# Optimization experiments

Hardware: AMD Instinct MI355X
Metric: run time of the kernel (lower is better)

The kernel has to match this reference:

```python
import jax, jax.numpy as jnp
import numpy as np

C = 256
DK = C // 8  # query/key channels


def setup_inputs() -> dict:
    key = jax.random.key(0)
    ks = jax.random.split(key, 7)
    B, W, H = 4, 64, 64
    x = jax.random.normal(ks[0], (B, C, W, H), dtype=jnp.float32)
    s_in = 1.0 / np.sqrt(C)
    Wq = jax.random.normal(ks[1], (DK, C), dtype=jnp.float32) * s_in
    bq = jnp.zeros((DK,), dtype=jnp.float32)
    Wk = jax.random.normal(ks[2], (DK, C), dtype=jnp.float32) * s_in
    bk = jnp.zeros((DK,), dtype=jnp.float32)
    Wv = jax.random.normal(ks[3], (C, C), dtype=jnp.float32) * s_in
    bv = jnp.zeros((C,), dtype=jnp.float32)
    return {"x": x, "Wq": Wq, "bq": bq, "Wk": Wk, "bk": bk, "Wv": Wv, "bv": bv}


def reference(x, Wq, bq, Wk, bk, Wv, bv):
    B, Cc, W, H = x.shape
    N = W * H
    xf = x.reshape(B, Cc, N)  # (B, C, N) flattened spatial
    # 1x1 convs == channel matmuls
    q = jnp.einsum('dc,bcn->bnd', Wq, xf) + bq  # (B, N, DK)
    k = jnp.einsum('dc,bcn->bdn', Wk, xf) + bk[None, :, None]  # (B, DK, N)
    v = jnp.einsum('oc,bcn->bon', Wv, xf) + bv[None, :, None]  # (B, C, N)
    energy = jnp.einsum('bnd,bdm->bnm', q, k) / jnp.sqrt(jnp.float32(q.shape[-1]))
    attn = jax.nn.softmax(energy, axis=-1)  # (B, N, N)
    out = jnp.einsum('bcn,bmn->bcm', v, attn)  # v @ attn^T
    return out.reshape(B, Cc, W, H) + x
```

## Files before the change

### kernel.cpp

```cpp
#include <hip/hip_runtime.h>
#include <hip/hip_bf16.h>
#include <math.h>

#define BB 4
#define CC 256
#define DKK 32
#define NN 4096
#define QSCALE 0.2550181864060454f

typedef __attribute__((ext_vector_type(8))) __bf16 bf16x8;
typedef __attribute__((ext_vector_type(4))) __bf16 bf16x4;
typedef __attribute__((ext_vector_type(4))) float f32x4;
typedef __attribute__((ext_vector_type(16))) float f32x16;

#define XST 260
#define SCRST 33

__global__ __launch_bounds__(256, 2) void qkv_kernel(
    const float* __restrict__ x,
    const float* __restrict__ Wq, const float* __restrict__ bq,
    const float* __restrict__ Wk, const float* __restrict__ bk,
    const float* __restrict__ Wv, const float* __restrict__ bv,
    __bf16* __restrict__ qws, __bf16* __restrict__ kws, __bf16* __restrict__ vws)
{
    __shared__ __align__(16) unsigned char smem[16640];
    __bf16* xsT = (__bf16*)smem;
    float*  scr = (float*)smem;

    const int tid = threadIdx.x;
    const int w   = tid >> 6;
    const int l   = tid & 63;
    const int l15 = l & 15;
    const int lq  = l >> 4;
    const int n0  = blockIdx.x * 32;
    const int b   = blockIdx.y;

    {
        const int cb = tid >> 3;
        const int nf = (tid & 7) * 4;
        const float* xp = x + ((size_t)(b * CC) + cb) * NN + n0 + nf;
#pragma unroll
        for (int r = 0; r < 8; r++) {
            float4 v = *(const float4*)(xp + (size_t)r * 32 * NN);
            int c = r * 32 + cb;
            xsT[(nf + 0) * XST + c] = (__bf16)v.x;
            xsT[(nf + 1) * XST + c] = (__bf16)v.y;
            xsT[(nf + 2) * XST + c] = (__bf16)v.z;
            xsT[(nf + 3) * XST + c] = (__bf16)v.w;
        }
    }

    const float* wp[5];
#pragma unroll
    for (int ot = 0; ot < 5; ot++) {
        int ob = 80 * w + 16 * ot;
        const float* src = (ob < 32) ? (Wq + (size_t)ob * CC)
                         : (ob < 64) ? (Wk + (size_t)(ob - 32) * CC)
                                     : (Wv + (size_t)(ob - 64) * CC);
        wp[ot] = src + (size_t)l15 * CC;
    }

    float4 wc[5][2], wn[5][2];
#pragma unroll
    for (int ot = 0; ot < 5; ot++) {
        wc[ot][0] = *(const float4*)(wp[ot] + lq * 8);
        wc[ot][1] = *(const float4*)(wp[ot] + lq * 8 + 4);
    }

    __syncthreads();

    const f32x4 zf = {0.f, 0.f, 0.f, 0.f};
    f32x4 acc[5][2];
#pragma unroll
    for (int i = 0; i < 5; i++)
#pragma unroll
        for (int j = 0; j < 2; j++) acc[i][j] = zf;

#pragma unroll
    for (int ks = 0; ks < 8; ks++) {
        if (ks < 7) {
#pragma unroll
            for (int ot = 0; ot < 5; ot++) {
                wn[ot][0] = *(const float4*)(wp[ot] + (ks + 1) * 32 + lq * 8);
                wn[ot][1] = *(const float4*)(wp[ot] + (ks + 1) * 32 + lq * 8 + 4);
            }
        }
        bf16x8 bfr[2];
#pragma unroll
        for (int nt = 0; nt < 2; nt++) {
            bf16x4 lo = *(const bf16x4*)&xsT[(nt * 16 + l15) * XST + ks * 32 + lq * 8];
            bf16x4 hi = *(const bf16x4*)&xsT[(nt * 16 + l15) * XST + ks * 32 + lq * 8 + 4];
            bfr[nt] = __builtin_shufflevector(lo, hi, 0, 1, 2, 3, 4, 5, 6, 7);
        }
#pragma unroll
        for (int ot = 0; ot < 5; ot++) {
            bf16x8 af;
            af[0] = (__bf16)wc[ot][0].x; af[1] = (__bf16)wc[ot][0].y;
            af[2] = (__bf16)wc[ot][0].z; af[3] = (__bf16)wc[ot][0].w;
            af[4] = (__bf16)wc[ot][1].x; af[5] = (__bf16)wc[ot][1].y;
            af[6] = (__bf16)wc[ot][1].z; af[7] = (__bf16)wc[ot][1].w;
#pragma unroll
            for (int nt = 0; nt < 2; nt++)
                acc[ot][nt] = __builtin_amdgcn_mfma_f32_16x16x32_bf16(af, bfr[nt], acc[ot][nt], 0, 0, 0);
        }
        if (ks < 7) {
#pragma unroll
            for (int ot = 0; ot < 5; ot++) { wc[ot][0] = wn[ot][0]; wc[ot][1] = wn[ot][1]; }
        }
    }

    __syncthreads();

    __bf16* vchunk = vws + (size_t)b * CC * NN + (size_t)(n0 >> 5) * 8192;
#pragma unroll
    for (int ot = 0; ot < 5; ot++) {
        int ob = 80 * w + ot * 16;
#pragma unroll
        for (int nt = 0; nt < 2; nt++) {
#pragma unroll
            for (int r = 0; r < 4; r++) {
                int o = ob + lq * 4 + r;
                int n = nt * 16 + l15;
                float val = acc[ot][nt][r];
                if (ob >= 64) {
                    int c = o - 64;
                    vchunk[(c >> 5) * 1024 + nt * 512 + (c & 31) * 16 + l15] =
                        (__bf16)(val + bv[c]);
                } else if (ob < 32) {
                    scr[o * SCRST + n] = (val + bq[o]) * QSCALE;
                } else {
                    scr[o * SCRST + n] = val + bk[o - 32];
                }
            }
        }
    }
    __syncthreads();
    {
        int n  = tid >> 3;
        int d0 = (tid & 7) * 4;
        bf16x4 qv, kv;
#pragma unroll
        for (int j = 0; j < 4; j++) {
            qv[j] = (__bf16)scr[(d0 + j) * SCRST + n];
            kv[j] = (__bf16)scr[(32 + d0 + j) * SCRST + n];
        }
        size_t base = ((size_t)b * NN + n0 + n) * DKK + d0;
        *(bf16x4*)&qws[base] = qv;
        *(bf16x4*)&kws[base] = kv;
    }
}

#define PST 36
#define MST 68
#define PWSZ (64 * PST)

__global__ __launch_bounds__(256, 2) void attn_kernel(
    const __bf16* __restrict__ qb, const __bf16* __restrict__ kb,
    const __bf16* __restrict__ vt, const float* __restrict__ x,
    float* __restrict__ out)
{
    __shared__ __align__(16) unsigned char smem[38144];
    __bf16* pw   = (__bf16*)smem + (threadIdx.x >> 6) * 2 * PWSZ;
    float*  Ls   = (float*)(smem + 36864);
    float*  Linv = (float*)(smem + 37888);

    const int tid = threadIdx.x;
    const int w   = tid >> 6;
    const int l   = tid & 63;
    const int l15 = l & 15;
    const int lq  = l >> 4;
    const int l31 = l & 31;
    const int lh  = l >> 5;

    const int beta = blockIdx.x;
    const int b    = (beta >> 1) & 3;
    const int ch   = (beta >> 3) & 1;
    const int mt   = ((beta >> 4) << 1) | (beta & 1);
    const int m0   = mt * 64;

    const __bf16* qbb = qb + (size_t)b * NN * DKK;
    const __bf16* kbb = kb + (size_t)b * NN * DKK;
    const __bf16* vtb = vt + (size_t)b * CC * NN;

    bf16x8 qa[4];
#pragma unroll
    for (int af = 0; af < 4; af++)
        qa[af] = *(const bf16x8*)(qbb + (size_t)(m0 + af * 16 + l15) * DKK + lq * 8);

    const __bf16* kstrip = kbb + (size_t)(w * 32 + l15) * DKK + lq * 8;
    const __bf16* vstrip = vtb + (size_t)w * 8192 + (size_t)ch * 4096
                               + l31 * 16 + lh * 8;

    const f32x4  zf  = {0.f, 0.f, 0.f, 0.f};
    f32x16 acc32[2][4];
    {
        const f32x16 z16 = {0.f,0.f,0.f,0.f,0.f,0.f,0.f,0.f,
                            0.f,0.f,0.f,0.f,0.f,0.f,0.f,0.f};
#pragma unroll
        for (int i = 0; i < 2; i++)
#pragma unroll
            for (int j = 0; j < 4; j++) acc32[i][j] = z16;
    }
    float lacc[4] = {0.f, 0.f, 0.f, 0.f};

    bf16x8 kA0 = *(const bf16x8*)kstrip;
    bf16x8 kA1 = *(const bf16x8*)(kstrip + 16 * DKK);
#pragma unroll
    for (int af = 0; af < 4; af++) {
        f32x4 e0 = __builtin_amdgcn_mfma_f32_16x16x32_bf16(kA0, qa[af], zf, 0, 0, 0);
        f32x4 e1 = __builtin_amdgcn_mfma_f32_16x16x32_bf16(kA1, qa[af], zf, 0, 0, 0);
        bf16x4 p0, p1;
#pragma unroll
        for (int r = 0; r < 4; r++) {
            float v0 = __builtin_amdgcn_exp2f(e0[r]); lacc[af] += v0; p0[r] = (__bf16)v0;
            float v1 = __builtin_amdgcn_exp2f(e1[r]); lacc[af] += v1; p1[r] = (__bf16)v1;
        }
        *(bf16x4*)&pw[(af * 16 + l15) * PST + lq * 4]      = p0;
        *(bf16x4*)&pw[(af * 16 + l15) * PST + 16 + lq * 4] = p1;
    }
    kA0 = *(const bf16x8*)(kstrip + (size_t)128 * DKK);
    kA1 = *(const bf16x8*)(kstrip + (size_t)144 * DKK);

#pragma unroll 2
    for (int ic = 0; ic < 31; ic++) {
        const int cur = ic & 1;
        const __bf16* vch = vstrip + (size_t)ic * 32768;

        bf16x8 vf[4][2];
#pragma unroll
        for (int ct = 0; ct < 4; ct++) {
            vf[ct][0] = *(const bf16x8*)(vch + ct * 1024);
            vf[ct][1] = *(const bf16x8*)(vch + ct * 1024 + 512);
        }

        bf16x8 pf[2][2];
#pragma unroll
        for (int mt2 = 0; mt2 < 2; mt2++)
#pragma unroll
            for (int ks = 0; ks < 2; ks++) {
                const __bf16* pr = &pw[cur * PWSZ + (mt2 * 32 + l31) * PST + ks * 16 + lh * 8];
                bf16x4 plo = *(const bf16x4*)pr;
                bf16x4 phi = *(const bf16x4*)(pr + 4);
                pf[mt2][ks] = __builtin_shufflevector(plo, phi, 0, 1, 2, 3, 4, 5, 6, 7);
            }

#pragma unroll
        for (int af = 0; af < 4; af++) {
            f32x4 e0 = __builtin_amdgcn_mfma_f32_16x16x32_bf16(kA0, qa[af], zf, 0, 0, 0);
            f32x4 e1 = __builtin_amdgcn_mfma_f32_16x16x32_bf16(kA1, qa[af], zf, 0, 0, 0);
            bf16x4 p0, p1;
#pragma unroll
            for (int r = 0; r < 4; r++) {
                float v0 = __builtin_amdgcn_exp2f(e0[r]); lacc[af] += v0; p0[r] = (__bf16)v0;
                float v1 = __builtin_amdgcn_exp2f(e1[r]); lacc[af] += v1; p1[r] = (__bf16)v1;
            }
            *(bf16x4*)&pw[(cur ^ 1) * PWSZ + (af * 16 + l15) * PST + lq * 4]      = p0;
            *(bf16x4*)&pw[(cur ^ 1) * PWSZ + (af * 16 + l15) * PST + 16 + lq * 4] = p1;
        }
        kA0 = *(const bf16x8*)(kstrip + (size_t)(ic + 2) * 128 * DKK);
        kA1 = *(const bf16x8*)(kstrip + (size_t)((ic + 2) * 128 + 16) * DKK);

#pragma unroll
        for (int mt2 = 0; mt2 < 2; mt2++)
#pragma unroll
            for (int ct = 0; ct < 4; ct++) {
                acc32[mt2][ct] = __builtin_amdgcn_mfma_f32_32x32x16_bf16(
                    vf[ct][0], pf[mt2][0], acc32[mt2][ct], 0, 0, 0);
                acc32[mt2][ct] = __builtin_amdgcn_mfma_f32_32x32x16_bf16(
                    vf[ct][1], pf[mt2][1], acc32[mt2][ct], 0, 0, 0);
            }
    }

    {
        const __bf16* vch = vstrip + (size_t)31 * 32768;
        bf16x8 vf[4][2];
#pragma unroll
        for (int ct = 0; ct < 4; ct++) {
            vf[ct][0] = *(const bf16x8*)(vch + ct * 1024);
            vf[ct][1] = *(const bf16x8*)(vch + ct * 1024 + 512);
        }
        bf16x8 pf[2][2];
#pragma unroll
        for (int mt2 = 0; mt2 < 2; mt2++)
#pragma unroll
            for (int ks = 0; ks < 2; ks++) {
                const __bf16* pr = &pw[(31 & 1) * PWSZ + (mt2 * 32 + l31) * PST + ks * 16 + lh * 8];
                bf16x4 plo = *(const bf16x4*)pr;
                bf16x4 phi = *(const bf16x4*)(pr + 4);
                pf[mt2][ks] = __builtin_shufflevector(plo, phi, 0, 1, 2, 3, 4, 5, 6, 7);
            }
#pragma unroll
        for (int mt2 = 0; mt2 < 2; mt2++)
#pragma unroll
            for (int ct = 0; ct < 4; ct++) {
                acc32[mt2][ct] = __builtin_amdgcn_mfma_f32_32x32x16_bf16(
                    vf[ct][0], pf[mt2][0], acc32[mt2][ct], 0, 0, 0);
                acc32[mt2][ct] = __builtin_amdgcn_mfma_f32_32x32x16_bf16(
                    vf[ct][1], pf[mt2][1], acc32[mt2][ct], 0, 0, 0);
            }
    }

#pragma unroll
    for (int af = 0; af < 4; af++) {
        lacc[af] += __shfl_xor(lacc[af], 16, 64);
        lacc[af] += __shfl_xor(lacc[af], 32, 64);
    }
    if (lq == 0) {
#pragma unroll
        for (int af = 0; af < 4; af++) Ls[w * 64 + af * 16 + l15] = lacc[af];
    }
    __syncthreads();
    if (tid < 64)
        Linv[tid] = 1.0f / (Ls[tid] + Ls[64 + tid] + Ls[128 + tid] + Ls[192 + tid]);

    float* Ored = (float*)smem + w * (32 * MST);
#pragma unroll
    for (int q = 0; q < 4; q++) {
        if (q > 0) __syncthreads();
#pragma unroll
        for (int mt2 = 0; mt2 < 2; mt2++) {
#pragma unroll
            for (int reg = 0; reg < 16; reg++) {
                int row = (reg & 3) + 8 * (reg >> 2) + 4 * lh;
                Ored[row * MST + mt2 * 32 + l31] = acc32[mt2][q][reg];
            }
        }
        __syncthreads();
        const int cl  = tid >> 3;
        const int mi0 = (tid & 7) * 8;
        const float* Ob = (const float*)smem + cl * MST;
#pragma unroll
        for (int j = 0; j < 2; j++) {
            int mi = mi0 + 4 * j;
            f32x4 s = *(const f32x4*)&Ob[mi];
            s = s + *(const f32x4*)&Ob[1 * (32 * MST) + mi];
            s = s + *(const f32x4*)&Ob[2 * (32 * MST) + mi];
            s = s + *(const f32x4*)&Ob[3 * (32 * MST) + mi];
            f32x4 li = *(const f32x4*)&Linv[mi];
            int c = ch * 128 + q * 32 + cl;
            size_t gi = ((size_t)(b * CC + c)) * NN + m0 + mi;
            f32x4 xr = *(const f32x4*)&x[gi];
            *(f32x4*)&out[gi] = s * li + xr;
        }
    }
}

extern "C" void kernel_launch(void* const* d_in, const int* in_sizes, int n_in,
                              void* d_out, int out_size, void* d_ws, size_t ws_size,
                              hipStream_t stream) {
    const float* x  = (const float*)d_in[0];
    const float* Wq = (const float*)d_in[1];
    const float* bq = (const float*)d_in[2];
    const float* Wk = (const float*)d_in[3];
    const float* bk = (const float*)d_in[4];
    const float* Wv = (const float*)d_in[5];
    const float* bv = (const float*)d_in[6];
    float* out = (float*)d_out;

    __bf16* qws = (__bf16*)d_ws;
    __bf16* kws = qws + (size_t)BB * NN * DKK;
    __bf16* vws = kws + (size_t)BB * NN * DKK;

    qkv_kernel<<<dim3(128, BB), 256, 0, stream>>>(x, Wq, bq, Wk, bk, Wv, bv,
                                                  qws, kws, vws);
    attn_kernel<<<dim3(512), 256, 0, stream>>>(qws, kws, vws, x, out);
}
```

Measured before the change: 152.5 us.

## Keep softmax probabilities in registers by matching QK^T MFMA output to PV input layout

```diff
diff --git a/kernel.cpp b/kernel.cpp
--- a/kernel.cpp
+++ b/kernel.cpp
@@ -111,6 +111,7 @@
 
     __syncthreads();
 
+    const int voff = ((l15 >> 2) & 1) * 8 + (l15 & 3) + ((l15 >> 3) & 1) * 4;
     __bf16* vchunk = vws + (size_t)b * CC * NN + (size_t)(n0 >> 5) * 8192;
 #pragma unroll
     for (int ot = 0; ot < 5; ot++) {
@@ -124,7 +125,7 @@
                 float val = acc[ot][nt][r];
                 if (ob >= 64) {
                     int c = o - 64;
-                    vchunk[(c >> 5) * 1024 + nt * 512 + (c & 31) * 16 + l15] =
+                    vchunk[(c >> 5) * 1024 + nt * 512 + (c & 31) * 16 + voff] =
                         (__bf16)(val + bv[c]);
                 } else if (ob < 32) {
                     scr[o * SCRST + n] = (val + bq[o]) * QSCALE;
@@ -150,25 +151,20 @@
     }
 }
 
-#define PST 36
 #define MST 68
-#define PWSZ (64 * PST)
 
 __global__ __launch_bounds__(256, 2) void attn_kernel(
     const __bf16* __restrict__ qb, const __bf16* __restrict__ kb,
     const __bf16* __restrict__ vt, const float* __restrict__ x,
     float* __restrict__ out)
 {
-    __shared__ __align__(16) unsigned char smem[38144];
-    __bf16* pw   = (__bf16*)smem + (threadIdx.x >> 6) * 2 * PWSZ;
-    float*  Ls   = (float*)(smem + 36864);
-    float*  Linv = (float*)(smem + 37888);
+    __shared__ __align__(16) unsigned char smem[36096];
+    float* Ls   = (float*)(smem + 34816);
+    float* Linv = (float*)(smem + 35840);
 
     const int tid = threadIdx.x;
     const int w   = tid >> 6;
     const int l   = tid & 63;
-    const int l15 = l & 15;
-    const int lq  = l >> 4;
     const int l31 = l & 31;
     const int lh  = l >> 5;
 
@@ -182,48 +178,32 @@
     const __bf16* kbb = kb + (size_t)b * NN * DKK;
     const __bf16* vtb = vt + (size_t)b * CC * NN;
 
-    bf16x8 qa[4];
-#pragma unroll
-    for (int af = 0; af < 4; af++)
-        qa[af] = *(const bf16x8*)(qbb + (size_t)(m0 + af * 16 + l15) * DKK + lq * 8);
-
-    const __bf16* kstrip = kbb + (size_t)(w * 32 + l15) * DKK + lq * 8;
+    bf16x8 qa[2][2];
+#pragma unroll
+    for (int mt2 = 0; mt2 < 2; mt2++)
+#pragma unroll
+        for (int kc = 0; kc < 2; kc++)
+            qa[mt2][kc] = *(const bf16x8*)(qbb + (size_t)(m0 + mt2 * 32 + l31) * DKK
+                                           + kc * 16 + lh * 8);
+
+    const __bf16* kstrip = kbb + (size_t)(w * 32 + l31) * DKK + lh * 8;
     const __bf16* vstrip = vtb + (size_t)w * 8192 + (size_t)ch * 4096
                                + l31 * 16 + lh * 8;
 
-    const f32x4  zf  = {0.f, 0.f, 0.f, 0.f};
+    const f32x16 z16 = {0.f,0.f,0.f,0.f,0.f,0.f,0.f,0.f,
+                        0.f,0.f,0.f,0.f,0.f,0.f,0.f,0.f};
     f32x16 acc32[2][4];
-    {
-        const f32x16 z16 = {0.f,0.f,0.f,0.f,0.f,0.f,0.f,0.f,
-                            0.f,0.f,0.f,0.f,0.f,0.f,0.f,0.f};
-#pragma unroll
-        for (int i = 0; i < 2; i++)
-#pragma unroll
-            for (int j = 0; j < 4; j++) acc32[i][j] = z16;
-    }
-    float lacc[4] = {0.f, 0.f, 0.f, 0.f};
-
-    bf16x8 kA0 = *(const bf16x8*)kstrip;
-    bf16x8 kA1 = *(const bf16x8*)(kstrip + 16 * DKK);
-#pragma unroll
-    for (int af = 0; af < 4; af++) {
-        f32x4 e0 = __builtin_amdgcn_mfma_f32_16x16x32_bf16(kA0, qa[af], zf, 0, 0, 0);
-        f32x4 e1 = __builtin_amdgcn_mfma_f32_16x16x32_bf16(kA1, qa[af], zf, 0, 0, 0);
-        bf16x4 p0, p1;
-#pragma unroll
-        for (int r = 0; r < 4; r++) {
-            float v0 = __builtin_amdgcn_exp2f(e0[r]); lacc[af] += v0; p0[r] = (__bf16)v0;
-            float v1 = __builtin_amdgcn_exp2f(e1[r]); lacc[af] += v1; p1[r] = (__bf16)v1;
-        }
-        *(bf16x4*)&pw[(af * 16 + l15) * PST + lq * 4]      = p0;
-        *(bf16x4*)&pw[(af * 16 + l15) * PST + 16 + lq * 4] = p1;
-    }
-    kA0 = *(const bf16x8*)(kstrip + (size_t)128 * DKK);
-    kA1 = *(const bf16x8*)(kstrip + (size_t)144 * DKK);
+#pragma unroll
+    for (int i = 0; i < 2; i++)
+#pragma unroll
+        for (int j = 0; j < 4; j++) acc32[i][j] = z16;
+    float lacc[2] = {0.f, 0.f};
+
+    bf16x8 kf0 = *(const bf16x8*)kstrip;
+    bf16x8 kf1 = *(const bf16x8*)(kstrip + 16);
 
 #pragma unroll 2
-    for (int ic = 0; ic < 31; ic++) {
-        const int cur = ic & 1;
+    for (int ic = 0; ic < 32; ic++) {
         const __bf16* vch = vstrip + (size_t)ic * 32768;
 
         bf16x8 vf[4][2];
@@ -233,81 +213,43 @@
             vf[ct][1] = *(const bf16x8*)(vch + ct * 1024 + 512);
         }
 
-        bf16x8 pf[2][2];
-#pragma unroll
-        for (int mt2 = 0; mt2 < 2; mt2++)
-#pragma unroll
-            for (int ks = 0; ks < 2; ks++) {
-                const __bf16* pr = &pw[cur * PWSZ + (mt2 * 32 + l31) * PST + ks * 16 + lh * 8];
-                bf16x4 plo = *(const bf16x4*)pr;
-                bf16x4 phi = *(const bf16x4*)(pr + 4);
-                pf[mt2][ks] = __builtin_shufflevector(plo, phi, 0, 1, 2, 3, 4, 5, 6, 7);
-            }
-
-#pragma unroll
-        for (int af = 0; af < 4; af++) {
-            f32x4 e0 = __builtin_amdgcn_mfma_f32_16x16x32_bf16(kA0, qa[af], zf, 0, 0, 0);
-            f32x4 e1 = __builtin_amdgcn_mfma_f32_16x16x32_bf16(kA1, qa[af], zf, 0, 0, 0);
-            bf16x4 p0, p1;
-#pragma unroll
-            for (int r = 0; r < 4; r++) {
-                float v0 = __builtin_amdgcn_exp2f(e0[r]); lacc[af] += v0; p0[r] = (__bf16)v0;
-                float v1 = __builtin_amdgcn_exp2f(e1[r]); lacc[af] += v1; p1[r] = (__bf16)v1;
-            }
-            *(bf16x4*)&pw[(cur ^ 1) * PWSZ + (af * 16 + l15) * PST + lq * 4]      = p0;
-            *(bf16x4*)&pw[(cur ^ 1) * PWSZ + (af * 16 + l15) * PST + 16 + lq * 4] = p1;
-        }
-        kA0 = *(const bf16x8*)(kstrip + (size_t)(ic + 2) * 128 * DKK);
-        kA1 = *(const bf16x8*)(kstrip + (size_t)((ic + 2) * 128 + 16) * DKK);
-
-#pragma unroll
-        for (int mt2 = 0; mt2 < 2; mt2++)
-#pragma unroll
-            for (int ct = 0; ct < 4; ct++) {
-                acc32[mt2][ct] = __builtin_amdgcn_mfma_f32_32x32x16_bf16(
-                    vf[ct][0], pf[mt2][0], acc32[mt2][ct], 0, 0, 0);
-                acc32[mt2][ct] = __builtin_amdgcn_mfma_f32_32x32x16_bf16(
-                    vf[ct][1], pf[mt2][1], acc32[mt2][ct], 0, 0, 0);
-            }
-    }
-
-    {
-        const __bf16* vch = vstrip + (size_t)31 * 32768;
-        bf16x8 vf[4][2];
+        f32x16 e0 = __builtin_amdgcn_mfma_f32_32x32x16_bf16(kf0, qa[0][0], z16, 0, 0, 0);
+        e0 = __builtin_amdgcn_mfma_f32_32x32x16_bf16(kf1, qa[0][1], e0, 0, 0, 0);
+        f32x16 e1 = __builtin_amdgcn_mfma_f32_32x32x16_bf16(kf0, qa[1][0], z16, 0, 0, 0);
+        e1 = __builtin_amdgcn_mfma_f32_32x32x16_bf16(kf1, qa[1][1], e1, 0, 0, 0);
+
+        kf0 = *(const bf16x8*)(kstrip + (size_t)(ic + 1) * 128 * DKK);
+        kf1 = *(const bf16x8*)(kstrip + (size_t)(ic + 1) * 128 * DKK + 16);
+
+        bf16x8 pb0[2], pb1[2];
+#pragma unroll
+        for (int r = 0; r < 16; r++) {
+            float v = __builtin_amdgcn_exp2f(e0[r]);
+            lacc[0] += v;
+            pb0[r >> 3][r & 7] = (__bf16)v;
+        }
+#pragma unroll
+        for (int r = 0; r < 16; r++) {
+            float v = __builtin_amdgcn_exp2f(e1[r]);
+            lacc[1] += v;
+            pb1[r >> 3][r & 7] = (__bf16)v;
+        }
+
 #pragma unroll
         for (int ct = 0; ct < 4; ct++) {
-            vf[ct][0] = *(const bf16x8*)(vch + ct * 1024);
-            vf[ct][1] = *(const bf16x8*)(vch + ct * 1024 + 512);
-        }
-        bf16x8 pf[2][2];
-#pragma unroll
-        for (int mt2 = 0; mt2 < 2; mt2++)
-#pragma unroll
-            for (int ks = 0; ks < 2; ks++) {
-                const __bf16* pr = &pw[(31 & 1) * PWSZ + (mt2 * 32 + l31) * PST + ks * 16 + lh * 8];
-                bf16x4 plo = *(const bf16x4*)pr;
-                bf16x4 phi = *(const bf16x4*)(pr + 4);
-                pf[mt2][ks] = __builtin_shufflevector(plo, phi, 0, 1, 2, 3, 4, 5, 6, 7);
-            }
-#pragma unroll
-        for (int mt2 = 0; mt2 < 2; mt2++)
-#pragma unroll
-            for (int ct = 0; ct < 4; ct++) {
-                acc32[mt2][ct] = __builtin_amdgcn_mfma_f32_32x32x16_bf16(
-                    vf[ct][0], pf[mt2][0], acc32[mt2][ct], 0, 0, 0);
-                acc32[mt2][ct] = __builtin_amdgcn_mfma_f32_32x32x16_bf16(
-                    vf[ct][1], pf[mt2][1], acc32[mt2][ct], 0, 0, 0);
-            }
-    }
-
-#pragma unroll
-    for (int af = 0; af < 4; af++) {
-        lacc[af] += __shfl_xor(lacc[af], 16, 64);
-        lacc[af] += __shfl_xor(lacc[af], 32, 64);
-    }
-    if (lq == 0) {
-#pragma unroll
-        for (int af = 0; af < 4; af++) Ls[w * 64 + af * 16 + l15] = lacc[af];
+            acc32[0][ct] = __builtin_amdgcn_mfma_f32_32x32x16_bf16(vf[ct][0], pb0[0], acc32[0][ct], 0, 0, 0);
+            acc32[0][ct] = __builtin_amdgcn_mfma_f32_32x32x16_bf16(vf[ct][1], pb0[1], acc32[0][ct], 0, 0, 0);
+            acc32[1][ct] = __builtin_amdgcn_mfma_f32_32x32x16_bf16(vf[ct][0], pb1[0], acc32[1][ct], 0, 0, 0);
+            acc32[1][ct] = __builtin_amdgcn_mfma_f32_32x32x16_bf16(vf[ct][1], pb1[1], acc32[1][ct], 0, 0, 0);
+        }
+    }
+
+#pragma unroll
+    for (int mt2 = 0; mt2 < 2; mt2++)
+        lacc[mt2] += __shfl_xor(lacc[mt2], 32, 64);
+    if (lh == 0) {
+        Ls[w * 64 + l31]      = lacc[0];
+        Ls[w * 64 + 32 + l31] = lacc[1];
     }
     __syncthreads();
     if (tid < 64)
```

Result: no change. 154.8 us (+1.5%).
